# Performance work log

Measured on AMD Instinct MI355X. Metric: run time of the kernel, lower is better.

Reference implementation:

```python
import jax, jax.numpy as jnp
import numpy as np

TEMP = 0.2
LAM = 0.5
EPS = 1e-8

N, IN_SIZE, HID = 8192, 256, 128


def setup_inputs() -> dict:
    key = jax.random.key(0)
    k1, k2, k3, k4, k5 = jax.random.split(key, 5)
    z_mp = jax.random.normal(k1, (N, IN_SIZE), dtype=jnp.float32)
    z_sc = jax.random.normal(k2, (N, IN_SIZE), dtype=jnp.float32)
    # xavier-normal-ish init scale
    W1 = jax.random.normal(k3, (IN_SIZE, HID), dtype=jnp.float32) * (1.414 * (2.0 / (IN_SIZE + HID)) ** 0.5)
    b1 = jnp.zeros((HID,), dtype=jnp.float32)
    W2 = jax.random.normal(k4, (HID, HID), dtype=jnp.float32) * (1.414 * (2.0 / (HID + HID)) ** 0.5)
    b2 = jnp.zeros((HID,), dtype=jnp.float32)
    pos = jax.random.randint(k5, (N, N), 0, 2, dtype=jnp.int32)
    return {"z_mp": z_mp, "z_sc": z_sc, "W1": W1, "b1": b1, "W2": W2, "b2": b2, "pos": pos}


def _proj(z, W1, b1, W2, b2):
    # Linear -> ELU -> Linear
    return jax.nn.elu(z @ W1 + b1) @ W2 + b2


def _l2norm(z):
    # F.normalize(p=2, dim=1): torch uses clamp_min(eps) on the norm
    n = jnp.linalg.norm(z, axis=1, keepdims=True)
    return z / jnp.maximum(n, 1e-12)


def reference(z_mp, z_sc, W1, b1, W2, b2, pos):
    zp_sc = _proj(z_sc, W1, b1, W2, b2)
    zp_mp = _proj(z_mp, W1, b1, W2, b2)
    # exp(cosine similarity / temperature), dense N x N
    sim = jnp.exp(_l2norm(zp_mp) @ _l2norm(zp_sc).T / TEMP)  # [N, N] mp2sc
    mp2sc = sim / (jnp.sum(sim, axis=1, keepdims=True) + EPS)
    sc2mp = sim.T / (jnp.sum(sim, axis=0)[:, None] + EPS)
    posf = pos.astype(sim.dtype)
    lori_sc = -jnp.log(jnp.sum(sc2mp * posf, axis=-1) + EPS)
    lori_mp = -jnp.log(jnp.sum(mp2sc * posf, axis=-1) + EPS)
    ans = LAM * lori_mp + (1.0 - LAM) * lori_sc
    ans = jnp.where(jnp.isnan(ans) | jnp.isinf(ans), jnp.zeros((), ans.dtype), ans)
    return ans
```

## Files before the change

kernel.cpp:

```cpp
#include <hip/hip_runtime.h>
#include <math.h>

#define N_ROWS 8192
#define IN_SZ 256
#define HID 128
#define INV_TEMP 5.0f
#define EPSV 1e-8f

typedef short short8 __attribute__((ext_vector_type(8)));
typedef float f32x4 __attribute__((ext_vector_type(4)));

__device__ __forceinline__ ushort f2bf(float v) {
    unsigned b = __float_as_uint(v);
    return (ushort)((b + 0x7FFFu + ((b >> 16) & 1u)) >> 16);
}
__device__ __forceinline__ float bf2f(ushort u) {
    return __uint_as_float(((unsigned)u) << 16);
}

__global__ __launch_bounds__(256) void proj_norm_kernel(
    const float* __restrict__ z_mp, const float* __restrict__ z_sc,
    const float* __restrict__ W1, const float* __restrict__ b1,
    const float* __restrict__ W2, const float* __restrict__ b2,
    ushort* __restrict__ h_mp, ushort* __restrict__ l_mp,
    ushort* __restrict__ h_sc, ushort* __restrict__ l_sc)
{
    __shared__ float smem[10368];
    float* sZ  = smem;
    float* sW  = smem + 2176;
    float* sH  = smem;
    float* sW2 = smem + 4224;
    float* snorm = smem + 8320;

    const int t = threadIdx.x;
    const int tx = t & 15, ty = t >> 4;
    const int R0 = blockIdx.x * 32;
    const float* z = (blockIdx.y == 0) ? z_mp : z_sc;
    ushort* outH   = (blockIdx.y == 0) ? h_mp : h_sc;
    ushort* outL   = (blockIdx.y == 0) ? l_mp : l_sc;

    if (t < 32) snorm[t] = 0.f;

    float acc[2][8];
#pragma unroll
    for (int i = 0; i < 2; ++i)
#pragma unroll
        for (int j = 0; j < 8; ++j) acc[i][j] = 0.f;

    for (int ch = 0; ch < 4; ++ch) {
#pragma unroll
        for (int it = 0; it < 2; ++it) {
            int idx = it * 256 + t;
            int k4 = idx >> 5;
            int m  = idx & 31;
            float4 v = *(const float4*)(z + (size_t)(R0 + m) * IN_SZ + ch * 64 + k4 * 4);
            sZ[(k4 * 4 + 0) * 34 + m] = v.x;
            sZ[(k4 * 4 + 1) * 34 + m] = v.y;
            sZ[(k4 * 4 + 2) * 34 + m] = v.z;
            sZ[(k4 * 4 + 3) * 34 + m] = v.w;
        }
#pragma unroll
        for (int it = 0; it < 8; ++it) {
            int idx = it * 256 + t;
            int kk = idx >> 5;
            int c4 = idx & 31;
            *(float4*)(sW + kk * 128 + c4 * 4) =
                *(const float4*)(W1 + (size_t)(ch * 64 + kk) * HID + c4 * 4);
        }
        __syncthreads();
#pragma unroll 8
        for (int k = 0; k < 64; ++k) {
            float2 a = *(const float2*)(sZ + k * 34 + ty * 2);
            float4 b0 = *(float4*)(sW + k * 128 + tx * 4);
            float4 b1v = *(float4*)(sW + k * 128 + 64 + tx * 4);
            float av[2] = {a.x, a.y};
            float bv[8] = {b0.x, b0.y, b0.z, b0.w, b1v.x, b1v.y, b1v.z, b1v.w};
#pragma unroll
            for (int i = 0; i < 2; ++i)
#pragma unroll
                for (int j = 0; j < 8; ++j)
                    acc[i][j] = fmaf(av[i], bv[j], acc[i][j]);
        }
        __syncthreads();
    }

#pragma unroll
    for (int j = 0; j < 8; ++j) {
        int c = (j < 4) ? tx * 4 + j : 64 + tx * 4 + (j - 4);
        float bb = b1[c];
#pragma unroll
        for (int i = 0; i < 2; ++i) {
            float v = acc[i][j] + bb;
            v = (v > 0.f) ? v : expm1f(v);
            sH[c * 33 + ty * 2 + i] = v;
        }
    }

    float acc2[2][8];
#pragma unroll
    for (int i = 0; i < 2; ++i)
#pragma unroll
        for (int j = 0; j < 8; ++j) acc2[i][j] = 0.f;

    for (int ch2 = 0; ch2 < 4; ++ch2) {
#pragma unroll
        for (int it = 0; it < 4; ++it) {
            int idx = it * 256 + t;
            int kk = idx >> 5;
            int c4 = idx & 31;
            *(float4*)(sW2 + kk * 128 + c4 * 4) =
                *(const float4*)(W2 + (size_t)(ch2 * 32 + kk) * HID + c4 * 4);
        }
        __syncthreads();
#pragma unroll 8
        for (int k2 = 0; k2 < 32; ++k2) {
            float a0 = sH[(ch2 * 32 + k2) * 33 + ty * 2];
            float a1 = sH[(ch2 * 32 + k2) * 33 + ty * 2 + 1];
            float4 b0 = *(float4*)(sW2 + k2 * 128 + tx * 4);
            float4 b1v = *(float4*)(sW2 + k2 * 128 + 64 + tx * 4);
            float av[2] = {a0, a1};
            float bv[8] = {b0.x, b0.y, b0.z, b0.w, b1v.x, b1v.y, b1v.z, b1v.w};
#pragma unroll
            for (int i = 0; i < 2; ++i)
#pragma unroll
                for (int j = 0; j < 8; ++j)
                    acc2[i][j] = fmaf(av[i], bv[j], acc2[i][j]);
        }
        __syncthreads();
    }

#pragma unroll
    for (int j = 0; j < 8; ++j) {
        int c = (j < 4) ? tx * 4 + j : 64 + tx * 4 + (j - 4);
        float bb = b2[c];
#pragma unroll
        for (int i = 0; i < 2; ++i) acc2[i][j] += bb;
    }
#pragma unroll
    for (int i = 0; i < 2; ++i) {
        float p = 0.f;
#pragma unroll
        for (int j = 0; j < 8; ++j) p = fmaf(acc2[i][j], acc2[i][j], p);
        atomicAdd(&snorm[ty * 2 + i], p);
    }
    __syncthreads();
#pragma unroll
    for (int i = 0; i < 2; ++i) {
        int r = ty * 2 + i;
        float scale = 1.f / fmaxf(sqrtf(snorm[r]), 1e-12f);
#pragma unroll
        for (int half = 0; half < 2; ++half) {
            ushort4 h4, l4;
            ushort hu[4], lu[4];
#pragma unroll
            for (int j = 0; j < 4; ++j) {
                float v = acc2[i][half * 4 + j] * scale;
                ushort hb = f2bf(v);
                float lv = v - bf2f(hb);
                hu[j] = hb;
                lu[j] = f2bf(lv);
            }
            h4.x = hu[0]; h4.y = hu[1]; h4.z = hu[2]; h4.w = hu[3];
            l4.x = lu[0]; l4.y = lu[1]; l4.z = lu[2]; l4.w = lu[3];
            size_t off = (size_t)(R0 + r) * HID + half * 64 + tx * 4;
            *(ushort4*)(outH + off) = h4;
            *(ushort4*)(outL + off) = l4;
        }
    }
}

__global__ __launch_bounds__(256) void sim_mfma_kernel(
    const ushort* __restrict__ mh_, const ushort* __restrict__ ml_,
    const ushort* __restrict__ sh_, const ushort* __restrict__ sl_,
    const int* __restrict__ pos, float* __restrict__ sums)
{
    __shared__ float redR[128], redRP[128], redC[128], redCP[128];
    __shared__ float tbuf[4][16 * 68];

    const int t = threadIdx.x;
    const int lane = t & 63;
    const int wave = t >> 6;
    const int wr = wave >> 1, wc = wave & 1;
    const int I = blockIdx.y * 128;
    const int J = blockIdx.x * 128;
    const int r0 = wr * 64, c0 = wc * 64;
    const int lrow = lane & 15;
    const int quad = lane >> 4;

    if (t < 128) { redR[t] = 0.f; redRP[t] = 0.f; }
    else { redC[t - 128] = 0.f; redCP[t - 128] = 0.f; }
    __syncthreads();

    const short* mh = (const short*)mh_;
    const short* ml = (const short*)ml_;
    const short* sh = (const short*)sh_;
    const short* sl = (const short*)sl_;

    size_t aoff[4], boff[4];
#pragma unroll
    for (int s = 0; s < 4; ++s) {
        aoff[s] = (size_t)(I + r0 + s * 16 + lrow) * HID + quad * 8;
        boff[s] = (size_t)(J + c0 + s * 16 + lrow) * HID + quad * 8;
    }

    f32x4 acc[4][4];
#pragma unroll
    for (int si = 0; si < 4; ++si)
#pragma unroll
        for (int sj = 0; sj < 4; ++sj) acc[si][sj] = (f32x4)0.f;

#pragma unroll
    for (int ks = 0; ks < 4; ++ks) {
        short8 ah[4], al[4], bh[4], bl[4];
#pragma unroll
        for (int s = 0; s < 4; ++s) {
            ah[s] = *(const short8*)(mh + aoff[s] + ks * 32);
            al[s] = *(const short8*)(ml + aoff[s] + ks * 32);
            bh[s] = *(const short8*)(sh + boff[s] + ks * 32);
            bl[s] = *(const short8*)(sl + boff[s] + ks * 32);
        }
#pragma unroll
        for (int si = 0; si < 4; ++si)
#pragma unroll
            for (int sj = 0; sj < 4; ++sj) {
                acc[si][sj] = __builtin_amdgcn_mfma_f32_16x16x32_bf16(
                    ah[si], bh[sj], acc[si][sj], 0, 0, 0);
                acc[si][sj] = __builtin_amdgcn_mfma_f32_16x16x32_bf16(
                    ah[si], bl[sj], acc[si][sj], 0, 0, 0);
                acc[si][sj] = __builtin_amdgcn_mfma_f32_16x16x32_bf16(
                    al[si], bh[sj], acc[si][sj], 0, 0, 0);
            }
    }

#pragma unroll
    for (int si = 0; si < 4; ++si)
#pragma unroll
        for (int sj = 0; sj < 4; ++sj)
#pragma unroll
            for (int r = 0; r < 4; ++r)
                acc[si][sj][r] = __expf(acc[si][sj][r] * INV_TEMP);

#pragma unroll
    for (int sj = 0; sj < 4; ++sj) {
        int n = c0 + sj * 16 + lrow;
        float cs = 0.f, cp = 0.f;
#pragma unroll
        for (int si = 0; si < 4; ++si) {
            f32x4 v = acc[si][sj];
            cs += v[0] + v[1] + v[2] + v[3];
            const int4 p = *(const int4*)(pos + (size_t)(J + n) * N_ROWS
                                          + I + r0 + si * 16 + quad * 4);
            cp += (p.x ? v[0] : 0.f) + (p.y ? v[1] : 0.f)
                + (p.z ? v[2] : 0.f) + (p.w ? v[3] : 0.f);
        }
        cs += __shfl_xor(cs, 16); cs += __shfl_xor(cs, 32);
        cp += __shfl_xor(cp, 16); cp += __shfl_xor(cp, 32);
        if (lane < 16) {
            atomicAdd(&redC[c0 + sj * 16 + lane], cs);
            atomicAdd(&redCP[c0 + sj * 16 + lane], cp);
        }
    }

    float* tw = tbuf[wave];
#pragma unroll
    for (int si = 0; si < 4; ++si) {
#pragma unroll
        for (int sj = 0; sj < 4; ++sj)
#pragma unroll
            for (int r = 0; r < 4; ++r)
                tw[(quad * 4 + r) * 68 + sj * 16 + lrow] = acc[si][sj][r];
        int row = lane & 15;
        int chunk = lane >> 2 >> 2;
        const int* prow = pos + (size_t)(I + r0 + si * 16 + row) * N_ROWS
                        + J + c0 + chunk * 16;
        float rs = 0.f, rp = 0.f;
#pragma unroll
        for (int c4 = 0; c4 < 4; ++c4) {
            f32x4 v = *(const f32x4*)(tw + row * 68 + chunk * 16 + c4 * 4);
            const int4 p = *(const int4*)(prow + c4 * 4);
            rs += v[0] + v[1] + v[2] + v[3];
            rp += (p.x ? v[0] : 0.f) + (p.y ? v[1] : 0.f)
                + (p.z ? v[2] : 0.f) + (p.w ? v[3] : 0.f);
        }
        rs += __shfl_xor(rs, 16); rs += __shfl_xor(rs, 32);
        rp += __shfl_xor(rp, 16); rp += __shfl_xor(rp, 32);
        if (lane < 16) {
            atomicAdd(&redR[r0 + si * 16 + lane], rs);
            atomicAdd(&redRP[r0 + si * 16 + lane], rp);
        }
    }
    __syncthreads();

    if (t < 128) {
        atomicAdd(&sums[I + t],              redR[t]);
        atomicAdd(&sums[N_ROWS + I + t],     redRP[t]);
        atomicAdd(&sums[2 * N_ROWS + J + t], redC[t]);
        atomicAdd(&sums[3 * N_ROWS + J + t], redCP[t]);
    }
}

__global__ __launch_bounds__(256) void finish_kernel(
    const float* __restrict__ sums, float* __restrict__ out)
{
    int i = blockIdx.x * 256 + threadIdx.x;
    if (i >= N_ROWS) return;
    float rsv = sums[i];
    float rpv = sums[N_ROWS + i];
    float csv = sums[2 * N_ROWS + i];
    float cpv = sums[3 * N_ROWS + i];
    float lmp = -logf(rpv / (rsv + EPSV) + EPSV);
    float lsc = -logf(cpv / (csv + EPSV) + EPSV);
    float a = 0.5f * lmp + 0.5f * lsc;
    if (!isfinite(a)) a = 0.f;
    out[i] = a;
}

extern "C" void kernel_launch(void* const* d_in, const int* in_sizes, int n_in,
                              void* d_out, int out_size, void* d_ws, size_t ws_size,
                              hipStream_t stream) {
    const float* z_mp = (const float*)d_in[0];
    const float* z_sc = (const float*)d_in[1];
    const float* W1   = (const float*)d_in[2];
    const float* b1   = (const float*)d_in[3];
    const float* W2   = (const float*)d_in[4];
    const float* b2   = (const float*)d_in[5];
    const int*   pos  = (const int*)d_in[6];
    float* out = (float*)d_out;

    ushort* wsu = (ushort*)d_ws;
    const size_t NV = (size_t)N_ROWS * HID;
    ushort* mh = wsu;
    ushort* ml = wsu + NV;
    ushort* sh = wsu + 2 * NV;
    ushort* sl = wsu + 3 * NV;
    float* sums = (float*)(wsu + 4 * NV);

    hipMemsetAsync(sums, 0, (size_t)4 * N_ROWS * sizeof(float), stream);
    proj_norm_kernel<<<dim3(N_ROWS / 32, 2), 256, 0, stream>>>(
        z_mp, z_sc, W1, b1, W2, b2, mh, ml, sh, sl);
    sim_mfma_kernel<<<dim3(64, 64), 256, 0, stream>>>(mh, ml, sh, sl, pos, sums);
    finish_kernel<<<N_ROWS / 256, 256, 0, stream>>>(sums, out);
}
```

Measured before the change: 529.8 us.

## Pack pos matrix into bitmask in prep kernel, read bits in sim kernel

Adds a packing phase, merged into the projection kernel as extra blocks, that converts the int32 N×N pos matrix into a 1-bit-per-entry bitmask using wave ballots. The sim kernel then loads 128-bit bitmask slices into shared memory instead of reading pos twice, once row-wise and once column-wise, at 32 bits per entry. The intent is to cut the sim kernel's dominant DRAM traffic. The packing pass still reads pos once, and the projection kernel also switches expm1f to __expf-1 and lowers its unroll factors.

```diff
diff --git a/kernel.cpp b/kernel.cpp
--- a/kernel.cpp
+++ b/kernel.cpp
@@ -6,6 +6,8 @@
 #define HID 128
 #define INV_TEMP 5.0f
 #define EPSV 1e-8f
+#define PACK_BLOCKS 2048
+#define PROJ_BLOCKS 512
 
 typedef short short8 __attribute__((ext_vector_type(8)));
 typedef float f32x4 __attribute__((ext_vector_type(4)));
@@ -18,7 +20,8 @@
     return __uint_as_float(((unsigned)u) << 16);
 }
 
-__global__ __launch_bounds__(256) void proj_norm_kernel(
+__global__ __launch_bounds__(256) void prep_kernel(
+    const int* __restrict__ pos, unsigned* __restrict__ posbits,
     const float* __restrict__ z_mp, const float* __restrict__ z_sc,
     const float* __restrict__ W1, const float* __restrict__ b1,
     const float* __restrict__ W2, const float* __restrict__ b2,
@@ -26,18 +29,45 @@
     ushort* __restrict__ h_sc, ushort* __restrict__ l_sc)
 {
     __shared__ float smem[10368];
+
+    const int t = threadIdx.x;
+
+    if (blockIdx.x < PACK_BLOCKS) {
+        const int lane = t & 63;
+        const int wave = t >> 6;
+        const int row = blockIdx.x * 4 + wave;
+        const int* prow = pos + (size_t)row * N_ROWS;
+        unsigned* orow = posbits + (size_t)row * (N_ROWS / 32);
+        for (int g = 0; g < 32; ++g) {
+            const int base = g * 256;
+            unsigned long long b0 = __ballot(prow[base + lane] != 0);
+            unsigned long long b1v = __ballot(prow[base + 64 + lane] != 0);
+            unsigned long long b2v = __ballot(prow[base + 128 + lane] != 0);
+            unsigned long long b3 = __ballot(prow[base + 192 + lane] != 0);
+            if (lane < 8) {
+                int which = lane >> 1;
+                unsigned long long m = (which == 0) ? b0 : (which == 1) ? b1v
+                                     : (which == 2) ? b2v : b3;
+                unsigned w = (lane & 1) ? (unsigned)(m >> 32) : (unsigned)m;
+                orow[g * 8 + lane] = w;
+            }
+        }
+        return;
+    }
+
     float* sZ  = smem;
     float* sW  = smem + 2176;
     float* sH  = smem;
     float* sW2 = smem + 4224;
     float* snorm = smem + 8320;
 
-    const int t = threadIdx.x;
+    const int id = blockIdx.x - PACK_BLOCKS;
+    const int sel = id >> 8;
+    const int R0 = (id & 255) * 32;
     const int tx = t & 15, ty = t >> 4;
-    const int R0 = blockIdx.x * 32;
-    const float* z = (blockIdx.y == 0) ? z_mp : z_sc;
-    ushort* outH   = (blockIdx.y == 0) ? h_mp : h_sc;
-    ushort* outL   = (blockIdx.y == 0) ? l_mp : l_sc;
+    const float* z = (sel == 0) ? z_mp : z_sc;
+    ushort* outH   = (sel == 0) ? h_mp : h_sc;
+    ushort* outL   = (sel == 0) ? l_mp : l_sc;
 
     if (t < 32) snorm[t] = 0.f;
 
@@ -68,7 +98,7 @@
                 *(const float4*)(W1 + (size_t)(ch * 64 + kk) * HID + c4 * 4);
         }
         __syncthreads();
-#pragma unroll 8
+#pragma unroll 4
         for (int k = 0; k < 64; ++k) {
             float2 a = *(const float2*)(sZ + k * 34 + ty * 2);
             float4 b0 = *(float4*)(sW + k * 128 + tx * 4);
@@ -91,7 +121,7 @@
 #pragma unroll
         for (int i = 0; i < 2; ++i) {
             float v = acc[i][j] + bb;
-            v = (v > 0.f) ? v : expm1f(v);
+            v = (v > 0.f) ? v : (__expf(v) - 1.f);
             sH[c * 33 + ty * 2 + i] = v;
         }
     }
@@ -112,7 +142,7 @@
                 *(const float4*)(W2 + (size_t)(ch2 * 32 + kk) * HID + c4 * 4);
         }
         __syncthreads();
-#pragma unroll 8
+#pragma unroll 4
         for (int k2 = 0; k2 < 32; ++k2) {
             float a0 = sH[(ch2 * 32 + k2) * 33 + ty * 2];
             float a1 = sH[(ch2 * 32 + k2) * 33 + ty * 2 + 1];
@@ -172,10 +202,12 @@
 __global__ __launch_bounds__(256) void sim_mfma_kernel(
     const ushort* __restrict__ mh_, const ushort* __restrict__ ml_,
     const ushort* __restrict__ sh_, const ushort* __restrict__ sl_,
-    const int* __restrict__ pos, float* __restrict__ sums)
+    const unsigned* __restrict__ posbits, float* __restrict__ sums)
 {
     __shared__ float redR[128], redRP[128], redC[128], redCP[128];
     __shared__ float tbuf[4][16 * 68];
+    __shared__ unsigned sBR[128][4];
+    __shared__ unsigned sBC[128][4];
 
     const int t = threadIdx.x;
     const int lane = t & 63;
@@ -187,8 +219,14 @@
     const int lrow = lane & 15;
     const int quad = lane >> 4;
 
-    if (t < 128) { redR[t] = 0.f; redRP[t] = 0.f; }
-    else { redC[t - 128] = 0.f; redCP[t - 128] = 0.f; }
+    if (t < 128) {
+        redR[t] = 0.f; redRP[t] = 0.f;
+        *(uint4*)sBR[t] = *(const uint4*)(posbits + (size_t)(I + t) * (N_ROWS / 32) + J / 32);
+    } else {
+        int u = t - 128;
+        redC[u] = 0.f; redCP[u] = 0.f;
+        *(uint4*)sBC[u] = *(const uint4*)(posbits + (size_t)(J + u) * (N_ROWS / 32) + I / 32);
+    }
     __syncthreads();
 
     const short* mh = (const short*)mh_;
@@ -248,10 +286,10 @@
         for (int si = 0; si < 4; ++si) {
             f32x4 v = acc[si][sj];
             cs += v[0] + v[1] + v[2] + v[3];
-            const int4 p = *(const int4*)(pos + (size_t)(J + n) * N_ROWS
-                                          + I + r0 + si * 16 + quad * 4);
-            cp += (p.x ? v[0] : 0.f) + (p.y ? v[1] : 0.f)
-                + (p.z ? v[2] : 0.f) + (p.w ? v[3] : 0.f);
+            int bb = r0 + si * 16 + quad * 4;
+            unsigned bits = (sBC[n][bb >> 5] >> (bb & 31)) & 0xF;
+            cp += (bits & 1u ? v[0] : 0.f) + (bits & 2u ? v[1] : 0.f)
+                + (bits & 4u ? v[2] : 0.f) + (bits & 8u ? v[3] : 0.f);
         }
         cs += __shfl_xor(cs, 16); cs += __shfl_xor(cs, 32);
         cp += __shfl_xor(cp, 16); cp += __shfl_xor(cp, 32);
@@ -270,17 +308,16 @@
             for (int r = 0; r < 4; ++r)
                 tw[(quad * 4 + r) * 68 + sj * 16 + lrow] = acc[si][sj][r];
         int row = lane & 15;
-        int chunk = lane >> 2 >> 2;
-        const int* prow = pos + (size_t)(I + r0 + si * 16 + row) * N_ROWS
-                        + J + c0 + chunk * 16;
+        int chunk = lane >> 4;
+        const unsigned prw = sBR[r0 + si * 16 + row][(c0 >> 5) + (chunk >> 1)];
         float rs = 0.f, rp = 0.f;
 #pragma unroll
         for (int c4 = 0; c4 < 4; ++c4) {
             f32x4 v = *(const f32x4*)(tw + row * 68 + chunk * 16 + c4 * 4);
-            const int4 p = *(const int4*)(prow + c4 * 4);
+            unsigned bits = (prw >> ((chunk & 1) * 16 + c4 * 4)) & 0xF;
             rs += v[0] + v[1] + v[2] + v[3];
-            rp += (p.x ? v[0] : 0.f) + (p.y ? v[1] : 0.f)
-                + (p.z ? v[2] : 0.f) + (p.w ? v[3] : 0.f);
+            rp += (bits & 1u ? v[0] : 0.f) + (bits & 2u ? v[1] : 0.f)
+                + (bits & 4u ? v[2] : 0.f) + (bits & 8u ? v[3] : 0.f);
         }
         rs += __shfl_xor(rs, 16); rs += __shfl_xor(rs, 32);
         rp += __shfl_xor(rp, 16); rp += __shfl_xor(rp, 32);
@@ -334,10 +371,11 @@
     ushort* sh = wsu + 2 * NV;
     ushort* sl = wsu + 3 * NV;
     float* sums = (float*)(wsu + 4 * NV);
+    unsigned* posbits = (unsigned*)(sums + 4 * N_ROWS);
 
     hipMemsetAsync(sums, 0, (size_t)4 * N_ROWS * sizeof(float), stream);
-    proj_norm_kernel<<<dim3(N_ROWS / 32, 2), 256, 0, stream>>>(
-        z_mp, z_sc, W1, b1, W2, b2, mh, ml, sh, sl);
-    sim_mfma_kernel<<<dim3(64, 64), 256, 0, stream>>>(mh, ml, sh, sl, pos, sums);
+    prep_kernel<<<PACK_BLOCKS + PROJ_BLOCKS, 256, 0, stream>>>(
+        pos, posbits, z_mp, z_sc, W1, b1, W2, b2, mh, ml, sh, sl);
+    sim_mfma_kernel<<<dim3(64, 64), 256, 0, stream>>>(mh, ml, sh, sl, posbits, sums);
     finish_kernel<<<N_ROWS / 256, 256, 0, stream>>>(sums, out);
 }
```

Result: slower. 551.6 us (+4.1%).
